# Performance work log

Measured on AMD Instinct MI355X. Metric: run time of the kernel, lower is better.

The kernel has to match this reference:

```python
import jax, jax.numpy as jnp
import numpy as np

NUM_ITEMS = 100000
NUM_ENTITIES = 1000000
EMBED_DIM = 64
BATCH = 16384
NUM_NEIGHBORS = 50


def setup_inputs() -> dict:
    key = jax.random.key(0)
    k1, k2, k3, k4, k5, k6 = jax.random.split(key, 6)
    item_indices = jax.random.randint(k1, (BATCH,), 0, NUM_ITEMS, dtype=jnp.int32)
    neighbor_indices = jax.random.randint(k2, (BATCH, NUM_NEIGHBORS), 0, NUM_ENTITIES, dtype=jnp.int32)
    item_table = jax.random.normal(k3, (NUM_ITEMS, EMBED_DIM), dtype=jnp.float32)
    entity_table = jax.random.normal(k4, (NUM_ENTITIES, EMBED_DIM), dtype=jnp.float32)
    # nn.Linear default init scale ~ 1/sqrt(fan_in)
    W = jax.random.uniform(k5, (EMBED_DIM, EMBED_DIM), dtype=jnp.float32, minval=-1.0, maxval=1.0) / jnp.sqrt(EMBED_DIM)
    b = jax.random.uniform(k6, (EMBED_DIM,), dtype=jnp.float32, minval=-1.0, maxval=1.0) / jnp.sqrt(EMBED_DIM)
    return {
        "item_indices": item_indices,
        "neighbor_indices": neighbor_indices,
        "item_table": item_table,
        "entity_table": entity_table,
        "W": W,
        "b": b,
    }


def reference(item_indices, neighbor_indices, item_table, entity_table, W, b):
    # [B, D] item embedding gather
    item_emb = item_table[item_indices]
    # [B, K, D] neighbor gather -> mean over K
    neighbor_emb = entity_table[neighbor_indices].mean(axis=1)
    x = item_emb + neighbor_emb
    # Linear + ReLU (dropout is identity in eval mode)
    x = jax.nn.relu(x @ W.T + b)
    return x
```

## Files before the change

### kernel.cpp

```cpp
#include <hip/hip_runtime.h>

#define EMBED_DIM 64
#define BATCH 16384
#define K_NBR 50

#define RPB 16
#define THREADS 256

__global__ __launch_bounds__(THREADS) void kgat_fused_kernel(
    const int* __restrict__ item_idx,
    const int* __restrict__ nbr_idx,
    const float* __restrict__ item_tab,
    const float* __restrict__ ent_tab,
    const float* __restrict__ W,
    const float* __restrict__ bias,
    float* __restrict__ out)
{
    __shared__ int   ids[RPB * K_NBR];
    __shared__ int   itid[RPB];
    __shared__ float xs[RPB][EMBED_DIM + 4];
    __shared__ float Wl[EMBED_DIM][EMBED_DIM + 1];

    const int t    = threadIdx.x;
    const int lane = t & 63;
    const int wave = t >> 6;
    const int row0 = blockIdx.x * RPB;

    #pragma unroll
    for (int i = t; i < EMBED_DIM * EMBED_DIM; i += THREADS)
        Wl[i >> 6][i & 63] = W[i];
    #pragma unroll
    for (int i = t; i < RPB * K_NBR; i += THREADS)
        ids[i] = nbr_idx[(size_t)row0 * K_NBR + i];
    if (t < RPB) itid[t] = item_idx[row0 + t];
    __syncthreads();

    {
        const int q = lane >> 4;
        const int c = lane & 15;
        const int r = wave * 4 + q;
        const int idbase = r * K_NBR;

        const float4* __restrict__ ent4  = (const float4*)ent_tab;
        const float4* __restrict__ item4 = (const float4*)item_tab;

        float4 acc = make_float4(0.f, 0.f, 0.f, 0.f);

        #pragma unroll 10
        for (int k = 0; k < K_NBR; ++k) {
            const int idx = ids[idbase + k];
            const float4 v = ent4[(size_t)idx * (EMBED_DIM / 4) + c];
            acc.x += v.x; acc.y += v.y; acc.z += v.z; acc.w += v.w;
        }

        const int it = itid[r];
        const float4 iv = item4[(size_t)it * (EMBED_DIM / 4) + c];
        const float s = 1.0f / K_NBR;
        float4 x;
        x.x = fmaf(acc.x, s, iv.x);
        x.y = fmaf(acc.y, s, iv.y);
        x.z = fmaf(acc.z, s, iv.z);
        x.w = fmaf(acc.w, s, iv.w);
        *(float4*)&xs[r][c * 4] = x;
    }

    __syncthreads();

    {
        const int j = lane;
        const int r0 = wave;
        float a0 = 0.f, a1 = 0.f, a2 = 0.f, a3 = 0.f;

        #pragma unroll
        for (int d = 0; d < EMBED_DIM; ++d) {
            const float w = Wl[j][d];
            a0 = fmaf(xs[r0     ][d], w, a0);
            a1 = fmaf(xs[r0 +  4][d], w, a1);
            a2 = fmaf(xs[r0 +  8][d], w, a2);
            a3 = fmaf(xs[r0 + 12][d], w, a3);
        }

        const float bb = bias[j];
        out[(size_t)(row0 + r0     ) * EMBED_DIM + j] = fmaxf(a0 + bb, 0.f);
        out[(size_t)(row0 + r0 +  4) * EMBED_DIM + j] = fmaxf(a1 + bb, 0.f);
        out[(size_t)(row0 + r0 +  8) * EMBED_DIM + j] = fmaxf(a2 + bb, 0.f);
        out[(size_t)(row0 + r0 + 12) * EMBED_DIM + j] = fmaxf(a3 + bb, 0.f);
    }
}

extern "C" void kernel_launch(void* const* d_in, const int* in_sizes, int n_in,
                              void* d_out, int out_size, void* d_ws, size_t ws_size,
                              hipStream_t stream) {
    const int*   item_idx = (const int*)  d_in[0];
    const int*   nbr_idx  = (const int*)  d_in[1];
    const float* item_tab = (const float*)d_in[2];
    const float* ent_tab  = (const float*)d_in[3];
    const float* W        = (const float*)d_in[4];
    const float* bias     = (const float*)d_in[5];
    float*       out      = (float*)      d_out;

    dim3 grid(BATCH / RPB);
    dim3 block(THREADS);
    kgat_fused_kernel<<<grid, block, 0, stream>>>(
        item_idx, nbr_idx, item_tab, ent_tab, W, bias, out);
}
```

Baseline: 40.92 us.

## Split neighbor reduction across two wave groups with 512-thread blocks

Doubles the block to 512 threads and splits the 50-neighbor gather sum into two halves, each handled by a group of four waves. The groups write partial sums to separate shared buffers, which are added during the linear layer. Each wave now computes two output rows instead of four. The aim is more memory parallelism and shorter per-thread gather chains, at the cost of more shared memory and extra shared-memory adds. The launch_bounds occupancy hint (8 blocks per SM) may also constrain register allocation.

```diff
diff --git a/kernel.cpp b/kernel.cpp
--- a/kernel.cpp
+++ b/kernel.cpp
@@ -5,9 +5,9 @@
 #define K_NBR 50
 
 #define RPB 16
-#define THREADS 256
+#define THREADS 512
 
-__global__ __launch_bounds__(THREADS) void kgat_fused_kernel(
+__global__ __launch_bounds__(THREADS, 8) void kgat_fused_kernel(
     const int* __restrict__ item_idx,
     const int* __restrict__ nbr_idx,
     const float* __restrict__ item_tab,
@@ -18,12 +18,14 @@
 {
     __shared__ int   ids[RPB * K_NBR];
     __shared__ int   itid[RPB];
-    __shared__ float xs[RPB][EMBED_DIM + 4];
+    __shared__ float xsp[2][RPB][EMBED_DIM + 4];
     __shared__ float Wl[EMBED_DIM][EMBED_DIM + 1];
 
     const int t    = threadIdx.x;
     const int lane = t & 63;
     const int wave = t >> 6;
+    const int g    = wave >> 2;
+    const int w    = wave & 3;
     const int row0 = blockIdx.x * RPB;
 
     #pragma unroll
@@ -38,30 +40,36 @@
     {
         const int q = lane >> 4;
         const int c = lane & 15;
-        const int r = wave * 4 + q;
+        const int r = w * 4 + q;
         const int idbase = r * K_NBR;
+        const int k0 = g * (K_NBR / 2);
+        const int k1 = k0 + (K_NBR / 2);
 
         const float4* __restrict__ ent4  = (const float4*)ent_tab;
         const float4* __restrict__ item4 = (const float4*)item_tab;
 
         float4 acc = make_float4(0.f, 0.f, 0.f, 0.f);
 
-        #pragma unroll 10
-        for (int k = 0; k < K_NBR; ++k) {
+        #pragma unroll 5
+        for (int k = k0; k < k1; ++k) {
             const int idx = ids[idbase + k];
             const float4 v = ent4[(size_t)idx * (EMBED_DIM / 4) + c];
             acc.x += v.x; acc.y += v.y; acc.z += v.z; acc.w += v.w;
         }
 
-        const int it = itid[r];
-        const float4 iv = item4[(size_t)it * (EMBED_DIM / 4) + c];
         const float s = 1.0f / K_NBR;
         float4 x;
-        x.x = fmaf(acc.x, s, iv.x);
-        x.y = fmaf(acc.y, s, iv.y);
-        x.z = fmaf(acc.z, s, iv.z);
-        x.w = fmaf(acc.w, s, iv.w);
-        *(float4*)&xs[r][c * 4] = x;
+        if (g == 0) {
+            const int it = itid[r];
+            const float4 iv = item4[(size_t)it * (EMBED_DIM / 4) + c];
+            x.x = fmaf(acc.x, s, iv.x);
+            x.y = fmaf(acc.y, s, iv.y);
+            x.z = fmaf(acc.z, s, iv.z);
+            x.w = fmaf(acc.w, s, iv.w);
+        } else {
+            x.x = acc.x * s; x.y = acc.y * s; x.z = acc.z * s; x.w = acc.w * s;
+        }
+        *(float4*)&xsp[g][r][c * 4] = x;
     }
 
     __syncthreads();
@@ -69,22 +77,20 @@
     {
         const int j = lane;
         const int r0 = wave;
-        float a0 = 0.f, a1 = 0.f, a2 = 0.f, a3 = 0.f;
+        float a0 = 0.f, a1 = 0.f;
 
         #pragma unroll
         for (int d = 0; d < EMBED_DIM; ++d) {
-            const float w = Wl[j][d];
-            a0 = fmaf(xs[r0     ][d], w, a0);
-            a1 = fmaf(xs[r0 +  4][d], w, a1);
-            a2 = fmaf(xs[r0 +  8][d], w, a2);
-            a3 = fmaf(xs[r0 + 12][d], w, a3);
+            const float wv = Wl[j][d];
+            const float x0 = xsp[0][r0    ][d] + xsp[1][r0    ][d];
+            const float x1 = xsp[0][r0 + 8][d] + xsp[1][r0 + 8][d];
+            a0 = fmaf(x0, wv, a0);
+            a1 = fmaf(x1, wv, a1);
         }
 
         const float bb = bias[j];
-        out[(size_t)(row0 + r0     ) * EMBED_DIM + j] = fmaxf(a0 + bb, 0.f);
-        out[(size_t)(row0 + r0 +  4) * EMBED_DIM + j] = fmaxf(a1 + bb, 0.f);
-        out[(size_t)(row0 + r0 +  8) * EMBED_DIM + j] = fmaxf(a2 + bb, 0.f);
-        out[(size_t)(row0 + r0 + 12) * EMBED_DIM + j] = fmaxf(a3 + bb, 0.f);
+        out[(size_t)(row0 + r0    ) * EMBED_DIM + j] = fmaxf(a0 + bb, 0.f);
+        out[(size_t)(row0 + r0 + 8) * EMBED_DIM + j] = fmaxf(a1 + bb, 0.f);
     }
 }
 
```

Measured after the change: 41.07 us. No clear change (+0.4%).
